# Kernel tuning notes

Measured on AMD Instinct MI355X. Metric: run time of the kernel, lower is better.

The kernel has to match this reference:

```python
import jax, jax.numpy as jnp
import numpy as np

WS = 5    # window_size
NH = 8    # num_heads
C = 96    # channels
LOG_MAX = float(np.log(1.0 / 0.01))  # clamp max for logit scales


def _conv3x3(x, w, b):
    # NCHW conv, stride 1, padding 1 ('SAME' for 3x3)
    y = jax.lax.conv_general_dilated(x, w, window_strides=(1, 1), padding='SAME',
                                     dimension_numbers=('NCHW', 'OIHW', 'NCHW'))
    return y + b[None, :, None, None]


def _l2norm(x):
    # matches F.normalize(dim=-1): x / max(||x||, 1e-12)
    n = jnp.linalg.norm(x, axis=-1, keepdims=True)
    return x / jnp.maximum(n, 1e-12)


def _wa(f, x, logit_scale):
    # f: (b, c, h, w); x: (b, 2c, h, w) -> windowed cosine attention
    b, c2, h, w = x.shape
    c = f.shape[1]
    hd = c // NH
    H, W = h // WS, w // WS
    # q: b (nh hd) (H ws) (W ws) -> (b H W) nh (ws ws) hd
    q = f.reshape(b, NH, hd, H, WS, W, WS).transpose(0, 3, 5, 1, 4, 6, 2)
    q = q.reshape(b * H * W, NH, WS * WS, hd)
    kv = x.reshape(b, 2, NH, hd, H, WS, W, WS).transpose(1, 0, 4, 6, 2, 5, 7, 3)
    kv = kv.reshape(2, b * H * W, NH, WS * WS, hd)
    k, v = kv[0], kv[1]
    scale = jnp.exp(jnp.minimum(logit_scale, LOG_MAX))  # (NH,1,1)
    atn = jnp.einsum('wnic,wnjc->wnij', _l2norm(q), _l2norm(k)) * scale[None]
    atn = jax.nn.softmax(atn, axis=-1)
    y = jnp.einsum('wnij,wnjc->wnic', atn, v)
    # back to (b, nh*hd, h, w)
    y = y.reshape(b, H, W, NH, WS, WS, hd).transpose(0, 3, 6, 1, 4, 2, 5)
    return y.reshape(b, c, h, w)


def reference(x, w_in, b_in, w_f, b_f, w_out, b_out, logit_scale, lr_logit_scale):
    b, c, h, w = x.shape
    xp = _conv3x3(x, w_in, b_in)   # (b, 2c, h, w)
    fp = _conv3x3(x, w_f, b_f)     # (b, c, h, w)
    sc2, sc = 2 * c // 3, c // 3
    xs = [xp[:, i * sc2:(i + 1) * sc2] for i in range(3)]
    fs = [fp[:, i * sc:(i + 1) * sc] for i in range(3)]
    ys = []
    # branch 0: plain window attention
    ys.append(_wa(fs[0], xs[0], logit_scale))
    # branch 1: shifted windows (torch rolls by -WS//2 = -3 and restores +WS//2 = +2)
    sh = -WS // 2  # Python: (-5)//2 = -3, matches torch code
    x_ = jnp.roll(xs[1], (sh, sh), axis=(2, 3))
    f_ = jnp.roll(fs[1], (sh, sh), axis=(2, 3))
    y_ = _wa(f_, x_, logit_scale)
    ys.append(jnp.roll(y_, (WS // 2, WS // 2), axis=(2, 3)))
    # branch 2: long-range axial (row then column) cosine attention
    hd = sc // NH
    q = fs[2].reshape(b, NH, hd, h, w).transpose(0, 1, 3, 4, 2)            # (b,n,h,w,c)
    kv = xs[2].reshape(b, 2, NH, hd, h, w).transpose(1, 0, 2, 4, 5, 3)      # (2,b,n,h,w,c)
    k, v = kv[0], kv[1]
    qn, kn = _l2norm(q), _l2norm(k)
    scale = jnp.exp(jnp.minimum(lr_logit_scale, LOG_MAX)).reshape(1, NH, 1, 1, 1)
    # row attention (over w)
    atn = jnp.einsum('bnhic,bnhjc->bnhij', qn, kn) * scale
    atn = jax.nn.softmax(atn, axis=-1)
    v = jnp.einsum('bnhij,bnhjc->bnhic', atn, v)
    # column attention (over h), reusing normalized q/k and same scale
    atn = jnp.einsum('bniwc,bnjwc->bnwij', qn, kn) * scale
    atn = jax.nn.softmax(atn, axis=-1)
    v = jnp.einsum('bnwij,bnjwc->bniwc', atn, v)
    ys.append(v.transpose(0, 1, 4, 2, 3).reshape(b, sc, h, w))
    y = jnp.concatenate(ys, axis=1)  # (b, c, h, w)
    return _conv3x3(y, w_out, b_out)


def setup_inputs() -> dict:
    key = jax.random.key(0)
    ks = jax.random.split(key, 8)
    B, H, W = 1, 240, 240
    inp = {
        'x': jax.random.normal(ks[0], (B, C, H, W), dtype=jnp.float32),
        'w_in': jax.random.normal(ks[1], (2 * C, C, 3, 3), dtype=jnp.float32) * 0.03,
        'b_in': jax.random.normal(ks[2], (2 * C,), dtype=jnp.float32) * 0.01,
        'w_f': jax.random.normal(ks[3], (C, C, 3, 3), dtype=jnp.float32) * 0.03,
        'b_f': jax.random.normal(ks[4], (C,), dtype=jnp.float32) * 0.01,
        'w_out': jax.random.normal(ks[5], (C, C, 3, 3), dtype=jnp.float32) * 0.03,
        'b_out': jax.random.normal(ks[6], (C,), dtype=jnp.float32) * 0.01,
        'logit_scale': jnp.log(10.0) * jnp.ones((NH, 1, 1), dtype=jnp.float32),
        'lr_logit_scale': jnp.log(10.0) * jnp.ones((NH, 1, 1), dtype=jnp.float32),
    }
    return inp
```

## Files before the change

### kernel.cpp

```cpp
#include <hip/hip_runtime.h>
#include <math.h>

#define HH 240
#define WW 240
#define PP (HH * WW)
#define PW 242
#define LOG_MAX_C 4.605170185988091f
#define LOG2E 1.442695040888963f

typedef __bf16 bf16x8 __attribute__((ext_vector_type(8)));
typedef float  f32x4  __attribute__((ext_vector_type(4)));

#define EXP2F(x) __builtin_amdgcn_exp2f(x)


__device__ __forceinline__ void to_xs_pad_body(
    int p, const float* __restrict__ in, __bf16* __restrict__ xs)
{
    if (p >= PW * PW) return;
    const int row = p / PW, px = p % PW;
    const bool border = (row == 0 || row == PW - 1 || px == 0 || px == PW - 1);
    union { __bf16 h[32]; uint4 u[4]; } pk;
#pragma unroll
    for (int icb = 0; icb < 3; ++icb) {
        uint4* op = (uint4*)(xs + (((size_t)row * 3 + icb) * PW + px) * 32);
        if (border) {
#pragma unroll
            for (int b = 0; b < 4; ++b) op[b] = make_uint4(0, 0, 0, 0);
        } else {
            const float* ip = in + (size_t)(icb * 32) * PP + (row - 1) * WW + (px - 1);
#pragma unroll
            for (int j = 0; j < 32; ++j) pk.h[j] = (__bf16)ip[(size_t)j * PP];
#pragma unroll
            for (int b = 0; b < 4; ++b) op[b] = pk.u[b];
        }
    }
}

__device__ __forceinline__ void wt_frag_body(
    int t, const float* __restrict__ w, __bf16* __restrict__ wtf, int OC)
{
    if (t >= 9 * (OC / 16) * 3 * 64) return;
    const int lane = t & 63;
    const int rest = t >> 6;
    const int icb  = rest % 3;
    const int to   = rest / 3;
    const int ocb  = to % (OC / 16);
    const int tap  = to / (OC / 16);
    const int ln = lane & 15, quad = lane >> 4;
    const int oc  = ocb * 16 + ln;
    const int ic0 = icb * 32 + quad * 8;
    __bf16* op = wtf + (size_t)rest * 512 + lane * 8;
#pragma unroll
    for (int d = 0; d < 8; ++d)
        op[d] = (__bf16)w[(size_t)(oc * 96 + ic0 + d) * 9 + tap];
}

__global__ __launch_bounds__(256) void prep_kernel(
    const float* __restrict__ x, const float* __restrict__ w_in,
    const float* __restrict__ w_f, const float* __restrict__ w_out,
    __bf16* __restrict__ xs, __bf16* __restrict__ wtf_in,
    __bf16* __restrict__ wtf_f, __bf16* __restrict__ wtf_o)
{
    const int bid = blockIdx.x, tid = threadIdx.x;
    if (bid < 81)       wt_frag_body(bid * 256 + tid, w_in, wtf_in, 192);
    else if (bid < 122) wt_frag_body((bid - 81) * 256 + tid, w_f, wtf_f, 96);
    else if (bid < 163) wt_frag_body((bid - 122) * 256 + tid, w_out, wtf_o, 96);
    else                to_xs_pad_body((bid - 163) * 256 + tid, x, xs);
}

template <int OC, int MT, int EPI>
__device__ __forceinline__ void conv_body(
    int bid, const __bf16* __restrict__ xs, const __bf16* __restrict__ wtf,
    const float* __restrict__ bias, float* __restrict__ out0,
    float* __restrict__ out1, const float* __restrict__ lsc,
    const float* __restrict__ lrlsc)
{
    const int group = bid / 24;
    const int w24   = bid % 24;
    const int z     = w24 >> 3;
    const int xy    = group * 8 + (w24 & 7);
    if (xy >= 450) return;
    const int x0  = (xy % 15) * 16;
    const int y0  = (xy / 15) * 8;
    const int oc0 = z * (MT * 16);
    const int ocb0 = oc0 / 16;

    const int wave = threadIdx.x >> 6;
    const int lane = threadIdx.x & 63;
    const int ln   = lane & 15;
    const int quad = lane >> 4;
    const int r0   = y0 + wave * 2;

    f32x4 acc[MT][2] = {};
    bf16x8 a[2][MT], b[2][2];

    const __bf16* abase = wtf + (size_t)lane * 8;
    const __bf16* bbase = xs + (size_t)ln * 32 + quad * 8;

#define LOAD_CHUNK(c, buf)                                                    \
    {                                                                         \
        const int tap_ = (c) / 3, icb_ = (c) % 3;                             \
        const int dy_ = tap_ / 3, dx_ = tap_ % 3;                             \
        const __bf16* ap_ = abase + (size_t)((tap_ * (OC / 16) + ocb0) * 3 + icb_) * 512; \
        _Pragma("unroll")                                                     \
        for (int mi = 0; mi < MT; ++mi)                                       \
            a[buf][mi] = *(const bf16x8*)(ap_ + (size_t)mi * 1536);           \
        _Pragma("unroll")                                                     \
        for (int ni = 0; ni < 2; ++ni)                                        \
            b[buf][ni] = *(const bf16x8*)(bbase +                             \
                (((size_t)(r0 + ni + dy_) * 3 + icb_) * PW + x0 + dx_) * 32); \
    }

    LOAD_CHUNK(0, 0)
#pragma unroll
    for (int c = 0; c < 27; ++c) {
        const int cur = c & 1, nxt = cur ^ 1;
        if (c < 26) LOAD_CHUNK(c + 1, nxt)
#pragma unroll
        for (int mi = 0; mi < MT; ++mi)
#pragma unroll
            for (int ni = 0; ni < 2; ++ni)
                acc[mi][ni] = __builtin_amdgcn_mfma_f32_16x16x32_bf16(
                    a[cur][mi], b[cur][ni], acc[mi][ni], 0, 0, 0);
    }
#undef LOAD_CHUNK

    if constexpr (EPI == 0) {
#pragma unroll
        for (int mi = 0; mi < MT; ++mi) {
#pragma unroll
            for (int r = 0; r < 4; ++r) {
                const int oc = oc0 + mi * 16 + quad * 4 + r;
                const float bv = bias[oc];
#pragma unroll
                for (int ni = 0; ni < 2; ++ni)
                    out0[(size_t)oc * PP + (r0 + ni) * WW + x0 + ln] = acc[mi][ni][r] + bv;
            }
        }
    } else if constexpr (EPI == 1) {
#pragma unroll
        for (int mi = 0; mi < MT; ++mi) {
            const f32x4 bv = *(const f32x4*)(bias + oc0 + mi * 16 + quad * 4);
            float* dst = (mi >> 1) ? out1 : out0;
            const int h8 = z * 8 + (mi & 1) * 4 + quad;
#pragma unroll
            for (int ni = 0; ni < 2; ++ni) {
                f32x4 o = acc[mi][ni] + bv;
                if ((mi >> 1) == 0) {
                    const float ksq = o[0]*o[0] + o[1]*o[1] + o[2]*o[2] + o[3]*o[3];
                    o *= 1.0f / fmaxf(sqrtf(ksq), 1e-12f);
                }
                *(f32x4*)(dst + (((size_t)h8 * 240 + r0 + ni) * 240 + x0 + ln) * 4) = o;
            }
        }
    } else {
#pragma unroll
        for (int mi = 0; mi < MT; ++mi) {
            const f32x4 bv = *(const f32x4*)(bias + oc0 + mi * 16 + quad * 4);
            const int h8 = z * 8 + mi * 4 + quad;
            const int br = h8 >> 3, hh = h8 & 7;
            const float ls = (br == 2) ? lrlsc[hh] : lsc[hh];
            const float qsc = __expf(fminf(ls, LOG_MAX_C)) * LOG2E;
#pragma unroll
            for (int ni = 0; ni < 2; ++ni) {
                f32x4 o = acc[mi][ni] + bv;
                const float qsq = o[0]*o[0] + o[1]*o[1] + o[2]*o[2] + o[3]*o[3];
                o *= qsc / fmaxf(sqrtf(qsq), 1e-12f);
                *(f32x4*)(out0 + (((size_t)h8 * 240 + r0 + ni) * 240 + x0 + ln) * 4) = o;
            }
        }
    }
}

__global__ __launch_bounds__(256) void conv_in_f(
    const __bf16* __restrict__ xs, const __bf16* __restrict__ wtf_in,
    const __bf16* __restrict__ wtf_f, const float* __restrict__ b_in,
    const float* __restrict__ b_f, float* __restrict__ xpk,
    float* __restrict__ xpv, float* __restrict__ fq4,
    const float* __restrict__ lsc, const float* __restrict__ lrlsc)
{
    const int bid = blockIdx.x;
    if (bid < 1368)
        conv_body<192, 4, 1>(bid, xs, wtf_in, b_in, xpk, xpv, nullptr, nullptr);
    else
        conv_body<96, 2, 2>(bid - 1368, xs, wtf_f, b_f, fq4, nullptr, lsc, lrlsc);
}

__global__ __launch_bounds__(256) void conv_out_k(
    const __bf16* __restrict__ ys, const __bf16* __restrict__ wtf_o,
    const float* __restrict__ b_out, float* __restrict__ out)
{
    conv_body<96, 2, 0>(blockIdx.x, ys, wtf_o, b_out, out, nullptr, nullptr, nullptr);
}

__global__ __launch_bounds__(256) void attn_row_fused(
    const float* __restrict__ fq4, const float* __restrict__ xpk,
    const float* __restrict__ xpv, const float* __restrict__ lsc,
    const float* __restrict__ lrlsc, __bf16* __restrict__ ys,
    float* __restrict__ v1)
{
    __shared__ f32x4 sm[960];
    const int bid = blockIdx.x;
    const int t = threadIdx.x;

    if (bid < 960) {
        const int bx = bid >> 3, h = bid & 7;
        const int half = t >> 7, tl = t & 127;
        const int y = bx * 2 + half;
        f32x4* ks = sm;
        f32x4* vs = sm + 480;

        const float scale = __expf(fminf(lrlsc[h], LOG_MAX_C));
        const float negM2 = -scale * LOG2E;
        const size_t rowb = ((size_t)h * 240 + y) * 240;
        const float* fq4b = fq4 + 64 * PP;
        const float* xpkb = xpk + 64 * PP;
        const float* xpvb = xpv + 64 * PP;
        f32x4 qreg[2] = {};

        if (tl < 120) {
#pragma unroll
            for (int s = 0; s < 2; ++s) {
                const int i = tl + s * 120;
                const size_t p4 = (rowb + i) * 4;
                ks[half * 240 + i] = *(const f32x4*)(xpkb + p4);
                vs[half * 240 + i] = *(const f32x4*)(xpvb + p4);
                qreg[s] = *(const f32x4*)(fq4b + p4);
            }
        }
        __syncthreads();
        if (tl < 120) {
            float l0 = 0.f, l1 = 0.f;
            f32x4 a0 = {0, 0, 0, 0}, a1 = {0, 0, 0, 0};
#pragma unroll 4
            for (int j = 0; j < 240; ++j) {
                const f32x4 kk = ks[half * 240 + j];
                const f32x4 vv = vs[half * 240 + j];
                const float s0 = fmaf(qreg[0][0], kk[0],
                                 fmaf(qreg[0][1], kk[1],
                                 fmaf(qreg[0][2], kk[2],
                                 fmaf(qreg[0][3], kk[3], negM2))));
                const float s1 = fmaf(qreg[1][0], kk[0],
                                 fmaf(qreg[1][1], kk[1],
                                 fmaf(qreg[1][2], kk[2],
                                 fmaf(qreg[1][3], kk[3], negM2))));
                const float p0 = EXP2F(s0);
                const float p1 = EXP2F(s1);
                l0 += p0; l1 += p1;
                a0 += vv * p0;
                a1 += vv * p1;
            }
            *(f32x4*)(v1 + (rowb + tl) * 4) = a0 * (1.0f / l0);
            *(f32x4*)(v1 + (rowb + tl + 120) * 4) = a1 * (1.0f / l1);
        }
    } else if (bid < 5568) {
        const int id2 = bid - 960;
        const int br  = id2 / 2304;
        const int id  = id2 % 2304;
        const int wi  = id / 288;
        const int g   = id % 288;
        const int wy  = g / 6;
        const int wx  = (g % 6) * 8 + wi;
        const int gshift = br * 3, sshift = br * 2;
        const size_t choff = (size_t)br * 32 * PP;
        const int h = t / 25, i = t % 25;
        f32x4* ks = sm;
        f32x4* vs = sm + 200;
        f32x4 qn = {0, 0, 0, 0};
        float negM2 = 0.f;
        int oy = 0, ox = 0;

        if (t < 200) {
            const int y = (wy * 5 + i / 5 + gshift) % HH;
            const int x = (wx * 5 + i % 5 + gshift) % WW;
            const size_t p4 = choff + (((size_t)h * 240 + y) * 240 + x) * 4;
            qn = *(const f32x4*)(fq4 + p4);
            ks[h * 25 + i] = *(const f32x4*)(xpk + p4);
            vs[h * 25 + i] = *(const f32x4*)(xpv + p4);
            const float scale = __expf(fminf(lsc[h], LOG_MAX_C));
            negM2 = -scale * LOG2E;
            oy = (wy * 5 + i / 5 + sshift) % HH;
            ox = (wx * 5 + i % 5 + sshift) % WW;
        }
        __syncthreads();
        if (t < 200) {
            float l = 0.f;
            f32x4 acc = {0, 0, 0, 0};
#pragma unroll
            for (int j = 0; j < 25; ++j) {
                const f32x4 kk = ks[h * 25 + j];
                const float s = fmaf(qn[0], kk[0],
                                fmaf(qn[1], kk[1],
                                fmaf(qn[2], kk[2],
                                fmaf(qn[3], kk[3], negM2))));
                const float p = EXP2F(s);
                l += p;
                acc += vs[h * 25 + j] * p;
            }
            const float linv = 1.0f / l;
            union { __bf16 h4[4]; uint2 u; } o;
#pragma unroll
            for (int d = 0; d < 4; ++d) o.h4[d] = (__bf16)(acc[d] * linv);
            *(uint2*)(ys + (((size_t)(oy + 1) * 3 + br) * PW + ox + 1) * 32 + h * 4) = o.u;
        }
    } else {
        const int idx = (bid - 5568) * 256 + t;
        if (idx >= 4 * PW) return;
        const int g = idx / PW, i = idx % PW;
        int row, px;
        if (g == 0)      { row = 0;      px = i; }
        else if (g == 1) { row = PW - 1; px = i; }
        else if (g == 2) { row = i;      px = 0; }
        else             { row = i;      px = PW - 1; }
#pragma unroll
        for (int icb = 0; icb < 3; ++icb) {
            uint4* op = (uint4*)(ys + (((size_t)row * 3 + icb) * PW + px) * 32);
#pragma unroll
            for (int b = 0; b < 4; ++b) op[b] = make_uint4(0, 0, 0, 0);
        }
    }
}

__global__ __launch_bounds__(256) void axial_col_kernel(
    const float* __restrict__ knb, const float* __restrict__ qnb,
    const float* __restrict__ v1b, const float* __restrict__ lsc,
    __bf16* __restrict__ ys)
{
    __shared__ f32x4 ks[2][240];
    __shared__ f32x4 vs[2][240];
    const int bid = blockIdx.x;
    const int wi  = bid / 120;
    const int g   = bid % 120;
    const int h   = g % 8;
    const int xc  = g / 8;
    const int t = threadIdx.x;
    const int half = t >> 7, tl = t & 127;
    const int x = xc * 16 + wi * 2 + half;

    const float scale = __expf(fminf(lsc[h], LOG_MAX_C));
    const float negM2 = -scale * LOG2E;
    const size_t hb = (size_t)h * 240;
    f32x4 qreg[2] = {};

    if (tl < 120) {
#pragma unroll
        for (int s = 0; s < 2; ++s) {
            const int i = tl + s * 120;
            const size_t p4 = ((hb + i) * 240 + x) * 4;
            ks[half][i] = *(const f32x4*)(knb + p4);
            vs[half][i] = *(const f32x4*)(v1b + p4);
            qreg[s] = *(const f32x4*)(qnb + p4);
        }
    }
    __syncthreads();
    if (tl < 120) {
        float l0 = 0.f, l1 = 0.f;
        f32x4 a0 = {0, 0, 0, 0}, a1 = {0, 0, 0, 0};
#pragma unroll 4
        for (int j = 0; j < 240; ++j) {
            const f32x4 kk = ks[half][j];
            const f32x4 vv = vs[half][j];
            const float s0 = fmaf(qreg[0][0], kk[0],
                             fmaf(qreg[0][1], kk[1],
                             fmaf(qreg[0][2], kk[2],
                             fmaf(qreg[0][3], kk[3], negM2))));
            const float s1 = fmaf(qreg[1][0], kk[0],
                             fmaf(qreg[1][1], kk[1],
                             fmaf(qreg[1][2], kk[2],
                             fmaf(qreg[1][3], kk[3], negM2))));
            const float p0 = EXP2F(s0);
            const float p1 = EXP2F(s1);
            l0 += p0; l1 += p1;
            a0 += vv * p0;
            a1 += vv * p1;
        }
#pragma unroll
        for (int s = 0; s < 2; ++s) {
            const f32x4 o4 = s ? a1 * (1.0f / l1) : a0 * (1.0f / l0);
            const int i = tl + s * 120;
            union { __bf16 h4[4]; uint2 u; } o;
#pragma unroll
            for (int d = 0; d < 4; ++d) o.h4[d] = (__bf16)o4[d];
            *(uint2*)(ys + (((size_t)(i + 1) * 3 + 2) * PW + x + 1) * 32 + h * 4) = o.u;
        }
    }
}

extern "C" void kernel_launch(void* const* d_in, const int* in_sizes, int n_in,
                              void* d_out, int out_size, void* d_ws, size_t ws_size,
                              hipStream_t stream)
{
    const float* x     = (const float*)d_in[0];
    const float* w_in  = (const float*)d_in[1];
    const float* b_in  = (const float*)d_in[2];
    const float* w_f   = (const float*)d_in[3];
    const float* b_f   = (const float*)d_in[4];
    const float* w_out = (const float*)d_in[5];
    const float* b_out = (const float*)d_in[6];
    const float* lsc   = (const float*)d_in[7];
    const float* lrlsc = (const float*)d_in[8];
    float* out = (float*)d_out;

    float* ws  = (float*)d_ws;
    float* xpk = ws;
    float* xpv = xpk + 96 * PP;
    float* fq4 = xpv + 96 * PP;
    __bf16* xs     = (__bf16*)(fq4 + 96 * PP);
    __bf16* wtf_in = xs + (size_t)PW * 3 * PW * 32;
    __bf16* wtf_f  = wtf_in + 9 * 12 * 3 * 512;
    __bf16* wtf_o  = wtf_f + 9 * 6 * 3 * 512;
    __bf16* ys     = xs;

    float* v1  = out;

    prep_kernel<<<392, 256, 0, stream>>>(x, w_in, w_f, w_out,
                                         xs, wtf_in, wtf_f, wtf_o);

    conv_in_f<<<2736, 256, 0, stream>>>(xs, wtf_in, wtf_f, b_in, b_f,
                                        xpk, xpv, fq4, lsc, lrlsc);

    attn_row_fused<<<5572, 256, 0, stream>>>(fq4, xpk, xpv, lsc, lrlsc, ys, v1);

    axial_col_kernel<<<960, 256, 0, stream>>>(
        xpk + 64 * PP, fq4 + 64 * PP, v1, lrlsc, ys);

    conv_out_k<<<1368, 256, 0, stream>>>(ys, wtf_o, b_out, out);
}
```

Measured before the change: 259.1 us.

## Merge five kernel launches into one persistent cooperative kernel with grid syncs

Replaces the five separate launches (prep, input convs, row/window attention, column attention, output conv) with one cooperative persistent kernel. Blocks loop over each stage's work items and a grid-wide barrier separates the stages. This is meant to remove per-launch overhead and the gaps between kernels. In exchange the grid is capped by occupancy (blocks per CU times 256), grid.sync adds barrier cost, and launch_bounds(256,4) may limit registers and cause spills in the conv bodies.

```diff
diff --git a/kernel.cpp b/kernel.cpp
--- a/kernel.cpp
+++ b/kernel.cpp
@@ -1,5 +1,8 @@
 #include <hip/hip_runtime.h>
+#include <hip/hip_cooperative_groups.h>
 #include <math.h>
+
+namespace cg = cooperative_groups;
 
 #define HH 240
 #define WW 240
@@ -54,19 +57,6 @@
 #pragma unroll
     for (int d = 0; d < 8; ++d)
         op[d] = (__bf16)w[(size_t)(oc * 96 + ic0 + d) * 9 + tap];
-}
-
-__global__ __launch_bounds__(256) void prep_kernel(
-    const float* __restrict__ x, const float* __restrict__ w_in,
-    const float* __restrict__ w_f, const float* __restrict__ w_out,
-    __bf16* __restrict__ xs, __bf16* __restrict__ wtf_in,
-    __bf16* __restrict__ wtf_f, __bf16* __restrict__ wtf_o)
-{
-    const int bid = blockIdx.x, tid = threadIdx.x;
-    if (bid < 81)       wt_frag_body(bid * 256 + tid, w_in, wtf_in, 192);
-    else if (bid < 122) wt_frag_body((bid - 81) * 256 + tid, w_f, wtf_f, 96);
-    else if (bid < 163) wt_frag_body((bid - 122) * 256 + tid, w_out, wtf_o, 96);
-    else                to_xs_pad_body((bid - 163) * 256 + tid, x, xs);
 }
 
 template <int OC, int MT, int EPI>
@@ -173,39 +163,17 @@
     }
 }
 
-__global__ __launch_bounds__(256) void conv_in_f(
-    const __bf16* __restrict__ xs, const __bf16* __restrict__ wtf_in,
-    const __bf16* __restrict__ wtf_f, const float* __restrict__ b_in,
-    const float* __restrict__ b_f, float* __restrict__ xpk,
-    float* __restrict__ xpv, float* __restrict__ fq4,
-    const float* __restrict__ lsc, const float* __restrict__ lrlsc)
-{
-    const int bid = blockIdx.x;
-    if (bid < 1368)
-        conv_body<192, 4, 1>(bid, xs, wtf_in, b_in, xpk, xpv, nullptr, nullptr);
-    else
-        conv_body<96, 2, 2>(bid - 1368, xs, wtf_f, b_f, fq4, nullptr, lsc, lrlsc);
-}
-
-__global__ __launch_bounds__(256) void conv_out_k(
-    const __bf16* __restrict__ ys, const __bf16* __restrict__ wtf_o,
-    const float* __restrict__ b_out, float* __restrict__ out)
-{
-    conv_body<96, 2, 0>(blockIdx.x, ys, wtf_o, b_out, out, nullptr, nullptr, nullptr);
-}
-
-__global__ __launch_bounds__(256) void attn_row_fused(
-    const float* __restrict__ fq4, const float* __restrict__ xpk,
+__device__ __forceinline__ void attn_body(
+    int item, const float* __restrict__ fq4, const float* __restrict__ xpk,
     const float* __restrict__ xpv, const float* __restrict__ lsc,
     const float* __restrict__ lrlsc, __bf16* __restrict__ ys,
-    float* __restrict__ v1)
-{
-    __shared__ f32x4 sm[960];
-    const int bid = blockIdx.x;
+    float* __restrict__ v1, f32x4* sm)
+{
     const int t = threadIdx.x;
-
-    if (bid < 960) {
-        const int bx = bid >> 3, h = bid & 7;
+    __syncthreads();
+
+    if (item < 960) {
+        const int bx = item >> 3, h = item & 7;
         const int half = t >> 7, tl = t & 127;
         const int y = bx * 2 + half;
         f32x4* ks = sm;
@@ -254,8 +222,8 @@
             *(f32x4*)(v1 + (rowb + tl) * 4) = a0 * (1.0f / l0);
             *(f32x4*)(v1 + (rowb + tl + 120) * 4) = a1 * (1.0f / l1);
         }
-    } else if (bid < 5568) {
-        const int id2 = bid - 960;
+    } else if (item < 5568) {
+        const int id2 = item - 960;
         const int br  = id2 / 2304;
         const int id  = id2 % 2304;
         const int wi  = id / 288;
@@ -305,7 +273,7 @@
             *(uint2*)(ys + (((size_t)(oy + 1) * 3 + br) * PW + ox + 1) * 32 + h * 4) = o.u;
         }
     } else {
-        const int idx = (bid - 5568) * 256 + t;
+        const int idx = (item - 5568) * 256 + t;
         if (idx >= 4 * PW) return;
         const int g = idx / PW, i = idx % PW;
         int row, px;
@@ -322,19 +290,20 @@
     }
 }
 
-__global__ __launch_bounds__(256) void axial_col_kernel(
-    const float* __restrict__ knb, const float* __restrict__ qnb,
+__device__ __forceinline__ void axial_col_body(
+    int item, const float* __restrict__ knb, const float* __restrict__ qnb,
     const float* __restrict__ v1b, const float* __restrict__ lsc,
-    __bf16* __restrict__ ys)
-{
-    __shared__ f32x4 ks[2][240];
-    __shared__ f32x4 vs[2][240];
-    const int bid = blockIdx.x;
-    const int wi  = bid / 120;
-    const int g   = bid % 120;
+    __bf16* __restrict__ ys, f32x4* sm)
+{
+    const int t = threadIdx.x;
+    __syncthreads();
+
+    f32x4* ks = sm;
+    f32x4* vs = sm + 480;
+    const int wi  = item / 120;
+    const int g   = item % 120;
     const int h   = g % 8;
     const int xc  = g / 8;
-    const int t = threadIdx.x;
     const int half = t >> 7, tl = t & 127;
     const int x = xc * 16 + wi * 2 + half;
 
@@ -348,8 +317,8 @@
         for (int s = 0; s < 2; ++s) {
             const int i = tl + s * 120;
             const size_t p4 = ((hb + i) * 240 + x) * 4;
-            ks[half][i] = *(const f32x4*)(knb + p4);
-            vs[half][i] = *(const f32x4*)(v1b + p4);
+            ks[half * 240 + i] = *(const f32x4*)(knb + p4);
+            vs[half * 240 + i] = *(const f32x4*)(v1b + p4);
             qreg[s] = *(const f32x4*)(qnb + p4);
         }
     }
@@ -359,8 +328,8 @@
         f32x4 a0 = {0, 0, 0, 0}, a1 = {0, 0, 0, 0};
 #pragma unroll 4
         for (int j = 0; j < 240; ++j) {
-            const f32x4 kk = ks[half][j];
-            const f32x4 vv = vs[half][j];
+            const f32x4 kk = ks[half * 240 + j];
+            const f32x4 vv = vs[half * 240 + j];
             const float s0 = fmaf(qreg[0][0], kk[0],
                              fmaf(qreg[0][1], kk[1],
                              fmaf(qreg[0][2], kk[2],
@@ -387,6 +356,61 @@
     }
 }
 
+__global__ __launch_bounds__(256, 4) void mega(
+    const float* __restrict__ x, const float* __restrict__ w_in,
+    const float* __restrict__ b_in, const float* __restrict__ w_f,
+    const float* __restrict__ b_f, const float* __restrict__ w_out,
+    const float* __restrict__ b_out, const float* __restrict__ lsc,
+    const float* __restrict__ lrlsc, float* __restrict__ out,
+    float* __restrict__ ws)
+{
+    __shared__ f32x4 sm[960];
+    float* xpk = ws;
+    float* xpv = xpk + 96 * PP;
+    float* fq4 = xpv + 96 * PP;
+    __bf16* xs     = (__bf16*)(fq4 + 96 * PP);
+    __bf16* wtf_in = xs + (size_t)PW * 3 * PW * 32;
+    __bf16* wtf_f  = wtf_in + 9 * 12 * 3 * 512;
+    __bf16* wtf_o  = wtf_f + 9 * 6 * 3 * 512;
+    __bf16* ys     = xs;
+    float* v1      = out;
+
+    const int nb = gridDim.x;
+    cg::grid_group grid = cg::this_grid();
+
+    for (int i = blockIdx.x; i < 392; i += nb) {
+        const int tid = threadIdx.x;
+        if (i < 81)       wt_frag_body(i * 256 + tid, w_in, wtf_in, 192);
+        else if (i < 122) wt_frag_body((i - 81) * 256 + tid, w_f, wtf_f, 96);
+        else if (i < 163) wt_frag_body((i - 122) * 256 + tid, w_out, wtf_o, 96);
+        else              to_xs_pad_body((i - 163) * 256 + tid, x, xs);
+    }
+    __threadfence();
+    grid.sync();
+
+    for (int i = blockIdx.x; i < 2736; i += nb) {
+        if (i < 1368)
+            conv_body<192, 4, 1>(i, xs, wtf_in, b_in, xpk, xpv, nullptr, nullptr);
+        else
+            conv_body<96, 2, 2>(i - 1368, xs, wtf_f, b_f, fq4, nullptr, lsc, lrlsc);
+    }
+    __threadfence();
+    grid.sync();
+
+    for (int i = blockIdx.x; i < 5572; i += nb)
+        attn_body(i, fq4, xpk, xpv, lsc, lrlsc, ys, v1, sm);
+    __threadfence();
+    grid.sync();
+
+    for (int i = blockIdx.x; i < 960; i += nb)
+        axial_col_body(i, xpk + 64 * PP, fq4 + 64 * PP, v1, lrlsc, ys, sm);
+    __threadfence();
+    grid.sync();
+
+    for (int i = blockIdx.x; i < 1368; i += nb)
+        conv_body<96, 2, 0>(i, ys, wtf_o, b_out, out, nullptr, nullptr, nullptr);
+}
+
 extern "C" void kernel_launch(void* const* d_in, const int* in_sizes, int n_in,
                               void* d_out, int out_size, void* d_ws, size_t ws_size,
                               hipStream_t stream)
@@ -401,29 +425,22 @@
     const float* lsc   = (const float*)d_in[7];
     const float* lrlsc = (const float*)d_in[8];
     float* out = (float*)d_out;
-
     float* ws  = (float*)d_ws;
-    float* xpk = ws;
-    float* xpv = xpk + 96 * PP;
-    float* fq4 = xpv + 96 * PP;
-    __bf16* xs     = (__bf16*)(fq4 + 96 * PP);
-    __bf16* wtf_in = xs + (size_t)PW * 3 * PW * 32;
-    __bf16* wtf_f  = wtf_in + 9 * 12 * 3 * 512;
-    __bf16* wtf_o  = wtf_f + 9 * 6 * 3 * 512;
-    __bf16* ys     = xs;
-
-    float* v1  = out;
-
-    prep_kernel<<<392, 256, 0, stream>>>(x, w_in, w_f, w_out,
-                                         xs, wtf_in, wtf_f, wtf_o);
-
-    conv_in_f<<<2736, 256, 0, stream>>>(xs, wtf_in, wtf_f, b_in, b_f,
-                                        xpk, xpv, fq4, lsc, lrlsc);
-
-    attn_row_fused<<<5572, 256, 0, stream>>>(fq4, xpk, xpv, lsc, lrlsc, ys, v1);
-
-    axial_col_kernel<<<960, 256, 0, stream>>>(
-        xpk + 64 * PP, fq4 + 64 * PP, v1, lrlsc, ys);
-
-    conv_out_k<<<1368, 256, 0, stream>>>(ys, wtf_o, b_out, out);
-}
+
+    static int ncoop = 0;
+    if (ncoop == 0) {
+        int nbpc = 0;
+        if (hipOccupancyMaxActiveBlocksPerMultiprocessor(&nbpc, mega, 256, 0)
+                != hipSuccess || nbpc < 1)
+            nbpc = 4;
+        if (nbpc > 8) nbpc = 8;
+        ncoop = nbpc * 256;
+    }
+
+    void* args[] = {
+        (void*)&x, (void*)&w_in, (void*)&b_in, (void*)&w_f, (void*)&b_f,
+        (void*)&w_out, (void*)&b_out, (void*)&lsc, (void*)&lrlsc,
+        (void*)&out, (void*)&ws
+    };
+    hipLaunchCooperativeKernel(mega, dim3(ncoop), dim3(256), args, 0, stream);
+}
```

Measured after the change: 801.9 us. +209.4%, slower.

## Stage conv weight fragments in shared memory, loaded once per block

Applied to the files above, without the earlier changes.

Until now every wave in the conv kernels loaded all MT weight fragments from global memory for each of the 27 chunks, so each block fetched the same weights four times. Now each of the first MT waves loads one fragment per chunk into a double-buffered shared-memory array, and all waves read their fragments from LDS. This cuts redundant global/L2 weight traffic. In exchange it adds a __syncthreads per chunk and LDS read latency on the critical path before the MFMAs.

```diff
diff --git a/kernel.cpp b/kernel.cpp
--- a/kernel.cpp
+++ b/kernel.cpp
@@ -74,7 +74,7 @@
     int bid, const __bf16* __restrict__ xs, const __bf16* __restrict__ wtf,
     const float* __restrict__ bias, float* __restrict__ out0,
     float* __restrict__ out1, const float* __restrict__ lsc,
-    const float* __restrict__ lrlsc)
+    const float* __restrict__ lrlsc, __bf16* As)
 {
     const int group = bid / 24;
     const int w24   = bid % 24;
@@ -93,38 +93,50 @@
     const int r0   = y0 + wave * 2;
 
     f32x4 acc[MT][2] = {};
-    bf16x8 a[2][MT], b[2][2];
+    bf16x8 a[MT], b[2][2], astg;
 
     const __bf16* abase = wtf + (size_t)lane * 8;
     const __bf16* bbase = xs + (size_t)ln * 32 + quad * 8;
 
-#define LOAD_CHUNK(c, buf)                                                    \
+#define ASRC(c) (abase + ((size_t)(((c) / 3) * (OC / 16) + ocb0 + wave) * 3 + (c) % 3) * 512)
+#define BLOAD(c, buf)                                                         \
     {                                                                         \
         const int tap_ = (c) / 3, icb_ = (c) % 3;                             \
         const int dy_ = tap_ / 3, dx_ = tap_ % 3;                             \
-        const __bf16* ap_ = abase + (size_t)((tap_ * (OC / 16) + ocb0) * 3 + icb_) * 512; \
-        _Pragma("unroll")                                                     \
-        for (int mi = 0; mi < MT; ++mi)                                       \
-            a[buf][mi] = *(const bf16x8*)(ap_ + (size_t)mi * 1536);           \
         _Pragma("unroll")                                                     \
         for (int ni = 0; ni < 2; ++ni)                                        \
             b[buf][ni] = *(const bf16x8*)(bbase +                             \
                 (((size_t)(r0 + ni + dy_) * 3 + icb_) * PW + x0 + dx_) * 32); \
     }
 
-    LOAD_CHUNK(0, 0)
+    if (wave < MT) {
+        astg = *(const bf16x8*)ASRC(0);
+        *(bf16x8*)(As + (size_t)wave * 512 + lane * 8) = astg;
+        astg = *(const bf16x8*)ASRC(1);
+    }
+    BLOAD(0, 0)
+
 #pragma unroll
     for (int c = 0; c < 27; ++c) {
         const int cur = c & 1, nxt = cur ^ 1;
-        if (c < 26) LOAD_CHUNK(c + 1, nxt)
+        __syncthreads();
+        if (c < 26 && wave < MT)
+            *(bf16x8*)(As + ((size_t)(nxt * MT) + wave) * 512 + lane * 8) = astg;
+#pragma unroll
+        for (int mi = 0; mi < MT; ++mi)
+            a[mi] = *(const bf16x8*)(As + ((size_t)(cur * MT) + mi) * 512 + lane * 8);
+        if (c < 25 && wave < MT)
+            astg = *(const bf16x8*)ASRC(c + 2);
+        if (c < 26) BLOAD(c + 1, nxt)
 #pragma unroll
         for (int mi = 0; mi < MT; ++mi)
 #pragma unroll
             for (int ni = 0; ni < 2; ++ni)
                 acc[mi][ni] = __builtin_amdgcn_mfma_f32_16x16x32_bf16(
-                    a[cur][mi], b[cur][ni], acc[mi][ni], 0, 0, 0);
-    }
-#undef LOAD_CHUNK
+                    a[mi], b[cur][ni], acc[mi][ni], 0, 0, 0);
+    }
+#undef ASRC
+#undef BLOAD
 
     if constexpr (EPI == 0) {
 #pragma unroll
@@ -180,18 +192,21 @@
     float* __restrict__ xpv, float* __restrict__ fq4,
     const float* __restrict__ lsc, const float* __restrict__ lrlsc)
 {
+    __shared__ __bf16 As[2 * 4 * 512];
     const int bid = blockIdx.x;
     if (bid < 1368)
-        conv_body<192, 4, 1>(bid, xs, wtf_in, b_in, xpk, xpv, nullptr, nullptr);
+        conv_body<192, 4, 1>(bid, xs, wtf_in, b_in, xpk, xpv, nullptr, nullptr, As);
     else
-        conv_body<96, 2, 2>(bid - 1368, xs, wtf_f, b_f, fq4, nullptr, lsc, lrlsc);
+        conv_body<96, 2, 2>(bid - 1368, xs, wtf_f, b_f, fq4, nullptr, lsc, lrlsc, As);
 }
 
 __global__ __launch_bounds__(256) void conv_out_k(
     const __bf16* __restrict__ ys, const __bf16* __restrict__ wtf_o,
     const float* __restrict__ b_out, float* __restrict__ out)
 {
-    conv_body<96, 2, 0>(blockIdx.x, ys, wtf_o, b_out, out, nullptr, nullptr, nullptr);
+    __shared__ __bf16 As[2 * 2 * 512];
+    conv_body<96, 2, 0>(blockIdx.x, ys, wtf_o, b_out, out, nullptr,
+                        nullptr, nullptr, As);
 }
 
 __global__ __launch_bounds__(256) void attn_row_fused(
```

Measured after the change: 230.9 us. 1.12x faster.
